# Kernel optimization log

Measured on AMD Instinct MI355X. Metric: run time of the kernel, lower is better.

Reference implementation:

```python
import math
import jax, jax.numpy as jnp
import numpy as np

S, B, H, D = 2048, 1, 16, 128  # seq, batch, heads, head_dim (hard-coded in source)
COEFF = 1.0  # layer_num = 1
NORM_FACTOR = math.sqrt(2048 / 16) * COEFF  # sqrt(HIDDEN/NUM_HEADS) * coeff


def setup_inputs() -> dict:
    key = jax.random.key(0)
    k1, k2, k3, k4, k5 = jax.random.split(key, 5)
    query_layer = jax.random.normal(k1, (S, B, H, D), dtype=jnp.float32)
    key_layer = jax.random.normal(k2, (S, B, H, D), dtype=jnp.float32)
    value_layer = jax.random.normal(k3, (S, B, H, D), dtype=jnp.float32)
    # causal mask, True = masked (Megatron convention)
    attention_mask = jnp.triu(jnp.ones((S, S), dtype=bool), k=1)[None, None]
    # per-head SVD right-singular-vector matrices (orthonormal-ish; random here)
    svd_qk = jax.random.normal(k4, (H, D, D), dtype=jnp.float32) / math.sqrt(D)
    svd_v = jax.random.normal(k5, (H, D, D), dtype=jnp.float32) / math.sqrt(D)
    return {"query_layer": query_layer, "key_layer": key_layer,
            "value_layer": value_layer, "attention_mask": attention_mask,
            "svd_qk": svd_qk, "svd_v": svd_v}


def reference(query_layer, key_layer, value_layer, attention_mask, svd_qk, svd_v):
    # q/k/v: [S, 1, H, D] -> project each head through its SVD matrix
    q = jnp.einsum('shd,hde->hse', query_layer[:, 0], svd_qk)  # [H,S,D]
    k = jnp.einsum('shd,hde->hse', key_layer[:, 0], svd_qk)    # [H,S,D]
    # qk_drop = 0 -> h_mask zeroing of columns is a no-op (faithfully skipped)
    scores = jnp.einsum('hqe,hke->hqk', q, k) / NORM_FACTOR    # [H,S,S]
    mask = attention_mask[0, 0]                                 # [S,S] bool
    scores = jnp.where(mask, jnp.float32(-10000.0), scores)
    # FusedScaleMaskSoftmax: scale by coeff, re-mask, softmax
    scaled = jnp.where(mask, jnp.float32(-10000.0), scores * COEFF)
    probs = jax.nn.softmax(scaled, axis=-1)                     # [H,S,S]
    # attention dropout is identity in eval mode
    v = jnp.einsum('shd,hde->hse', value_layer[:, 0], svd_v)    # [H,S,D]
    # vlinear_drop = 0 -> column zeroing is a no-op
    ctx = jnp.einsum('hqk,hke->qhe', probs, v)                  # [S,H,D]
    return ctx.reshape(S, B, H * D)                             # [S,1,2048]
```

## Files before the change

### kernel.cpp

```cpp
#include <hip/hip_runtime.h>
#include <hip/hip_bf16.h>
#include <math.h>

#define S_LEN 2048
#define NHEAD 16
#define DHEAD 128

typedef __attribute__((ext_vector_type(8)))  _Float16 f16x8;
typedef __attribute__((ext_vector_type(4)))  _Float16 f16x4;
typedef __attribute__((ext_vector_type(4)))  float    f32x4;
typedef __attribute__((ext_vector_type(16))) float    f32x16;

__device__ __forceinline__ void permswap(unsigned &a, unsigned &b) {
    asm volatile("v_permlane32_swap_b32 %0, %1" : "+v"(a), "+v"(b));
}

typedef __attribute__((address_space(3))) unsigned int lds_u32;
typedef __attribute__((address_space(1))) const unsigned int glb_u32;
__device__ __forceinline__ void gload16(const void* g, void* l) {
    __builtin_amdgcn_global_load_lds((glb_u32*)g, (lds_u32*)l, 16, 0, 0);
}

__global__ __launch_bounds__(256) void transpose_w_kernel(
    const float* __restrict__ w_qk, const float* __restrict__ w_v,
    _Float16* __restrict__ wqk_t, _Float16* __restrict__ wv_t)
{
    __shared__ float tile[32][33];
    const int mat = blockIdx.z;
    const int h   = blockIdx.y;
    const int t0  = blockIdx.x;
    const int dt  = (t0 >> 2) * 32;
    const int et  = (t0 & 3) * 32;
    const float* src = (mat ? w_v : w_qk) + (size_t)h * DHEAD * DHEAD;
    _Float16*   dst = (mat ? wv_t : wqk_t) + (size_t)h * DHEAD * DHEAD;
    const int tx = threadIdx.x & 31, ty = threadIdx.x >> 5;
#pragma unroll
    for (int k = 0; k < 4; ++k)
        tile[ty + 8 * k][tx] = src[(size_t)(dt + ty + 8 * k) * DHEAD + et + tx];
    __syncthreads();
#pragma unroll
    for (int k = 0; k < 4; ++k)
        dst[(size_t)(et + ty + 8 * k) * DHEAD + dt + tx] = (_Float16)tile[tx][ty + 8 * k];
}

__global__ __launch_bounds__(256) void proj_kernel(
    const float* __restrict__ q_in, const float* __restrict__ k_in,
    const float* __restrict__ v_in,
    const _Float16* __restrict__ wqk_t, const _Float16* __restrict__ wv_t,
    _Float16* __restrict__ Qp, _Float16* __restrict__ Kp, _Float16* __restrict__ Vt)
{
    const int h   = blockIdx.x >> 5;
    const int rb  = blockIdx.x & 31;
    const int wv  = threadIdx.x >> 6;
    const int lane = threadIdx.x & 63;
    const int r16 = lane & 15;
    const int kg  = lane >> 4;
    const int s_base = rb * 64 + wv * 16;
    const int s_row  = s_base + r16;
    const float INV_NORM = 0.08838834764831845f;

    f16x8 aq[4], ak[4], av[4];
    {
        const float* qr = q_in + ((size_t)s_row * NHEAD + h) * DHEAD;
        const float* kr = k_in + ((size_t)s_row * NHEAD + h) * DHEAD;
        const float* vr = v_in + ((size_t)s_row * NHEAD + h) * DHEAD;
#pragma unroll
        for (int kb = 0; kb < 4; ++kb) {
            const int d0 = kb * 32 + kg * 8;
            const f32x4 q0 = *(const f32x4*)(qr + d0), q1 = *(const f32x4*)(qr + d0 + 4);
            const f32x4 k0 = *(const f32x4*)(kr + d0), k1 = *(const f32x4*)(kr + d0 + 4);
            const f32x4 v0 = *(const f32x4*)(vr + d0), v1 = *(const f32x4*)(vr + d0 + 4);
#pragma unroll
            for (int i = 0; i < 4; ++i) {
                aq[kb][i] = (_Float16)q0[i];  aq[kb][i + 4] = (_Float16)q1[i];
                ak[kb][i] = (_Float16)k0[i];  ak[kb][i + 4] = (_Float16)k1[i];
                av[kb][i] = (_Float16)v0[i];  av[kb][i + 4] = (_Float16)v1[i];
            }
        }
    }

    const _Float16* wq_h = wqk_t + (size_t)h * DHEAD * DHEAD;
    const _Float16* wv_h = wv_t  + (size_t)h * DHEAD * DHEAD;

#pragma unroll 2
    for (int cb = 0; cb < 8; ++cb) {
        f32x4 accq = {0.f, 0.f, 0.f, 0.f};
        f32x4 acck = {0.f, 0.f, 0.f, 0.f};
        f32x4 accv = {0.f, 0.f, 0.f, 0.f};
        const int c = cb * 16 + r16;
#pragma unroll
        for (int kb = 0; kb < 4; ++kb) {
            const f16x8 bqk = *(const f16x8*)(wq_h + (size_t)c * DHEAD + kb * 32 + kg * 8);
            const f16x8 bv  = *(const f16x8*)(wv_h + (size_t)c * DHEAD + kb * 32 + kg * 8);
            accq = __builtin_amdgcn_mfma_f32_16x16x32_f16(bqk, aq[kb], accq, 0, 0, 0);
            acck = __builtin_amdgcn_mfma_f32_16x16x32_f16(bqk, ak[kb], acck, 0, 0, 0);
            accv = __builtin_amdgcn_mfma_f32_16x16x32_f16(av[kb], bv,  accv, 0, 0, 0);
        }
        f16x4 qv, kv4;
#pragma unroll
        for (int jj = 0; jj < 4; ++jj) {
            qv[jj]  = (_Float16)(accq[jj] * INV_NORM);
            kv4[jj] = (_Float16)acck[jj];
        }
        *(f16x4*)(Qp + ((size_t)h * S_LEN + s_base + r16) * DHEAD + cb * 16 + kg * 4) = qv;
        *(f16x4*)(Kp + ((size_t)h * S_LEN + s_base + r16) * DHEAD + cb * 16 + kg * 4) = kv4;
        f16x4 vvv;
#pragma unroll
        for (int jj = 0; jj < 4; ++jj) vvv[jj] = (_Float16)accv[jj];
        *(f16x4*)(Vt + ((size_t)h * DHEAD + c) * S_LEN + s_base + kg * 4) = vvv;
    }
}

__device__ __forceinline__ void stage_k(const _Float16* kbase, _Float16* kst,
                                        int w, int lane, int par, int inext,
                                        int jmax_lock) {
#pragma unroll
    for (int cidx = 0; cidx < 2; ++cidx) {
        const int c      = 2 * w + cidx;
        const int role_c = c >> 3;
        const int cc     = c & 7;
        const int jn     = 2 * inext + role_c;
        if (jn < jmax_lock) {
            const int A    = cc * 1024 + lane * 16;
            const int srcO = A ^ (((A >> 8) & 15) << 4);
            const char* g  = (const char*)kbase + (size_t)jn * 8192 + srcO;
            char*       l  = (char*)kst + (size_t)(role_c * 2 + par) * 8192
                                        + cc * 1024;
            gload16(g, l);
        }
    }
}

__global__ __launch_bounds__(512, 2) void attn_kernel(
    const _Float16* __restrict__ Qp, const _Float16* __restrict__ Kp,
    const _Float16* __restrict__ Vt, float* __restrict__ out)
{
    __shared__ _Float16 Kst[4][4096];
    __shared__ _Float16 obuf[4][32][132];
    __shared__ float    mlbuf[4][2][32];

    const int h    = blockIdx.y;
    const int w    = threadIdx.x >> 6;
    const int lane = threadIdx.x & 63;
    const int q    = lane & 31;
    const int hi   = lane >> 5;

    const int qsub = w & 1;
    const int role = (w >> 1) & 1;
    const int tsel = w >> 2;
    const int t    = tsel ? (31 - blockIdx.x) : blockIdx.x;
    const int pairid = qsub + tsel * 2;
    const int q0w  = t * 64 + qsub * 32;
    const int jmax = 2 * t + 1 + qsub;
    const int q_abs = q0w + q;

    const int jmax_lock = 2 * (31 - blockIdx.x) + 2;
    const int I         = jmax_lock / 2;

    const _Float16* qbase = Qp + ((size_t)h * S_LEN + q0w) * DHEAD;
    const _Float16* kbase = Kp + (size_t)h * S_LEN * DHEAD;
    const _Float16* vbase = Vt + (size_t)h * DHEAD * S_LEN;

    const int lqk = q * DHEAD + hi * 8;
    const int lv  = q * S_LEN + hi * 8;
    const int swq = (q & 15) << 4;

    f16x8 qf[8];
#pragma unroll
    for (int m = 0; m < 8; ++m)
        qf[m] = *(const f16x8*)(qbase + lqk + m * 16);

    f32x16 acc[4];
#pragma unroll
    for (int e = 0; e < 4; ++e)
#pragma unroll
        for (int i = 0; i < 16; ++i) acc[e][i] = 0.f;

    float m_run = -1e30f, l_run = 0.f;

    stage_k(kbase, &Kst[0][0], w, lane, 0, 0, jmax_lock);

    int p = 0;
    for (int it = 0; it < I; ++it, p ^= 1) {
        __syncthreads();

        const int j   = 2 * it + role;
        const bool act = (j < jmax);
        const int kv0 = j * 32;

        f16x8 kf[8];
        if (act) {
            const char* kt = (const char*)&Kst[role * 2 + p][0];
#pragma unroll
            for (int m = 0; m < 8; ++m) {
                const int L = q * 256 + m * 32 + hi * 16;
                kf[m] = *(const f16x8*)(kt + (L ^ swq));
            }
        }

        if (it + 1 < I)
            stage_k(kbase, &Kst[0][0], w, lane, p ^ 1, it + 1, jmax_lock);

        if (act) {
            f32x16 s0, s1;
#pragma unroll
            for (int i = 0; i < 16; ++i) { s0[i] = 0.f; s1[i] = 0.f; }
#pragma unroll
            for (int m = 0; m < 8; m += 2) {
                s0 = __builtin_amdgcn_mfma_f32_32x32x16_f16(kf[m],     qf[m],     s0, 0, 0, 0);
                s1 = __builtin_amdgcn_mfma_f32_32x32x16_f16(kf[m + 1], qf[m + 1], s1, 0, 0, 0);
            }

            f16x8 vf[8];
#pragma unroll
            for (int e = 0; e < 4; ++e) {
                const _Float16* vp = vbase + (size_t)e * 32 * S_LEN + lv + kv0;
                vf[2 * e]     = *(const f16x8*)(vp);
                vf[2 * e + 1] = *(const f16x8*)(vp + 16);
            }

            f32x16 sv = s0 + s1;

            if (kv0 == q0w) {
#pragma unroll
                for (int i = 0; i < 16; ++i) {
                    const int krel = (i & 3) + 8 * (i >> 2) + 4 * hi;
                    if (kv0 + krel > q_abs) sv[i] = -1e30f;
                }
            }

            float t0 = fmaxf(sv[0], sv[1]),  t1 = fmaxf(sv[2], sv[3]);
            float t2 = fmaxf(sv[4], sv[5]),  t3 = fmaxf(sv[6], sv[7]);
            float t4 = fmaxf(sv[8], sv[9]),  t5 = fmaxf(sv[10], sv[11]);
            float t6 = fmaxf(sv[12], sv[13]), t7 = fmaxf(sv[14], sv[15]);
            t0 = fmaxf(t0, t1); t2 = fmaxf(t2, t3); t4 = fmaxf(t4, t5); t6 = fmaxf(t6, t7);
            float tm = fmaxf(fmaxf(t0, t2), fmaxf(t4, t6));
            tm = fmaxf(tm, __shfl_xor(tm, 32, 64));

            const float mnew = fmaxf(m_run, tm);
            if (__any(tm > m_run)) {
                const float corr = __expf(m_run - mnew);
                l_run *= corr;
#pragma unroll
                for (int e = 0; e < 4; ++e)
#pragma unroll
                    for (int i = 0; i < 16; ++i) acc[e][i] *= corr;
                m_run = mnew;
            }

#pragma unroll
            for (int i = 0; i < 16; ++i) sv[i] = __expf(sv[i] - m_run);
            float r0 = (sv[0] + sv[1]) + (sv[2] + sv[3]);
            float r1 = (sv[4] + sv[5]) + (sv[6] + sv[7]);
            float r2 = (sv[8] + sv[9]) + (sv[10] + sv[11]);
            float r3 = (sv[12] + sv[13]) + (sv[14] + sv[15]);
            float rs = (r0 + r1) + (r2 + r3);
            rs += __shfl_xor(rs, 32, 64);
            l_run += rs;

            unsigned u0 = __builtin_bit_cast(unsigned, __builtin_amdgcn_cvt_pkrtz(sv[0],  sv[1]));
            unsigned u1 = __builtin_bit_cast(unsigned, __builtin_amdgcn_cvt_pkrtz(sv[2],  sv[3]));
            unsigned u2 = __builtin_bit_cast(unsigned, __builtin_amdgcn_cvt_pkrtz(sv[4],  sv[5]));
            unsigned u3 = __builtin_bit_cast(unsigned, __builtin_amdgcn_cvt_pkrtz(sv[6],  sv[7]));
            unsigned u4 = __builtin_bit_cast(unsigned, __builtin_amdgcn_cvt_pkrtz(sv[8],  sv[9]));
            unsigned u5 = __builtin_bit_cast(unsigned, __builtin_amdgcn_cvt_pkrtz(sv[10], sv[11]));
            unsigned u6 = __builtin_bit_cast(unsigned, __builtin_amdgcn_cvt_pkrtz(sv[12], sv[13]));
            unsigned u7 = __builtin_bit_cast(unsigned, __builtin_amdgcn_cvt_pkrtz(sv[14], sv[15]));
            permswap(u0, u2); permswap(u1, u3);
            permswap(u4, u6); permswap(u5, u7);
            union uf8 { unsigned w[4]; f16x8 v; };
            uf8 p0; p0.w[0] = u0; p0.w[1] = u1; p0.w[2] = u2; p0.w[3] = u3;
            uf8 p1; p1.w[0] = u4; p1.w[1] = u5; p1.w[2] = u6; p1.w[3] = u7;

#pragma unroll
            for (int e = 0; e < 4; ++e) {
                acc[e] = __builtin_amdgcn_mfma_f32_32x32x16_f16(vf[2 * e],     p0.v, acc[e], 0, 0, 0);
                acc[e] = __builtin_amdgcn_mfma_f32_32x32x16_f16(vf[2 * e + 1], p1.v, acc[e], 0, 0, 0);
            }
        }
    }

    if (role) {
        if (hi == 0) { mlbuf[pairid][0][q] = m_run; mlbuf[pairid][1][q] = l_run; }
#pragma unroll
        for (int e = 0; e < 4; ++e)
#pragma unroll
            for (int i = 0; i < 16; ++i) {
                const int erow = e * 32 + (i & 3) + 8 * (i >> 2) + 4 * hi;
                obuf[pairid][q][erow] = (_Float16)acc[e][i];
            }
    }
    __syncthreads();
    if (!role) {
        const float mb = mlbuf[pairid][0][q];
        const float lb = mlbuf[pairid][1][q];
        const float ms = fmaxf(m_run, mb);
        const float ca = __expf(m_run - ms);
        const float cb = __expf(mb - ms);
        const float rinv = 1.0f / (l_run * ca + lb * cb);
        float* orow = out + (size_t)q_abs * (NHEAD * DHEAD) + h * DHEAD;
#pragma unroll
        for (int e = 0; e < 4; ++e) {
#pragma unroll
            for (int g = 0; g < 4; ++g) {
                f32x4 vv;
#pragma unroll
                for (int c = 0; c < 4; ++c) {
                    const int i = g * 4 + c;
                    const int erow = e * 32 + 8 * g + 4 * hi + c;
                    vv[c] = (acc[e][i] * ca + (float)obuf[pairid][q][erow] * cb) * rinv;
                }
                *(f32x4*)(orow + e * 32 + 8 * g + 4 * hi) = vv;
            }
        }
    }
}

extern "C" void kernel_launch(void* const* d_in, const int* in_sizes, int n_in,
                              void* d_out, int out_size, void* d_ws, size_t ws_size,
                              hipStream_t stream) {
    const float* q_in = (const float*)d_in[0];
    const float* k_in = (const float*)d_in[1];
    const float* v_in = (const float*)d_in[2];
    const float* w_qk = (const float*)d_in[4];
    const float* w_v  = (const float*)d_in[5];
    float* out = (float*)d_out;

    const size_t mat_elems = (size_t)NHEAD * S_LEN * DHEAD;
    const size_t w_elems   = (size_t)NHEAD * DHEAD * DHEAD;
    _Float16* Qp   = (_Float16*)d_ws;
    _Float16* Kp   = Qp + mat_elems;
    _Float16* Vt   = Kp + mat_elems;
    _Float16* Wqkt = Vt + mat_elems;
    _Float16* Wvt  = Wqkt + w_elems;

    transpose_w_kernel<<<dim3(16, NHEAD, 2), dim3(256), 0, stream>>>(w_qk, w_v, Wqkt, Wvt);
    proj_kernel<<<dim3(NHEAD * 32), dim3(256), 0, stream>>>(q_in, k_in, v_in, Wqkt, Wvt, Qp, Kp, Vt);
    attn_kernel<<<dim3(16, NHEAD), dim3(512), 0, stream>>>(Qp, Kp, Vt, out);
}
```

Measured before the change: 92.44 us.

## Process two KV tiles per iteration per role and use exp2 softmax

Each wave now handles two 32-key tiles per loop iteration, and the K staging buffer grows to eight slots so each step loads four tiles. This halves the number of barriers and online-softmax rescale checks. The 1/sqrt(d) scale now includes log2(e), so the softmax uses exp2f instead of __expf. In exchange, LDS use and register pressure go up, which could lower occupancy at 2 blocks per CU, and the tile-granularity masking becomes a little coarser.

```diff
diff --git a/kernel.cpp b/kernel.cpp
--- a/kernel.cpp
+++ b/kernel.cpp
@@ -57,7 +57,7 @@
     const int kg  = lane >> 4;
     const int s_base = rb * 64 + wv * 16;
     const int s_row  = s_base + r16;
-    const float INV_NORM = 0.08838834764831845f;
+    const float INV_NORM = 0.12752211758f;
 
     f16x8 aq[4], ak[4], av[4];
     {
@@ -111,20 +111,20 @@
     }
 }
 
-__device__ __forceinline__ void stage_k(const _Float16* kbase, _Float16* kst,
-                                        int w, int lane, int par, int inext,
-                                        int jmax_lock) {
-#pragma unroll
-    for (int cidx = 0; cidx < 2; ++cidx) {
-        const int c      = 2 * w + cidx;
-        const int role_c = c >> 3;
-        const int cc     = c & 7;
-        const int jn     = 2 * inext + role_c;
+__device__ __forceinline__ void stage_k4(const _Float16* kbase, _Float16* kst,
+                                         int w, int lane, int par, int inext,
+                                         int jmax_lock) {
+#pragma unroll
+    for (int cidx = 0; cidx < 4; ++cidx) {
+        const int c    = 4 * w + cidx;
+        const int slot = c >> 3;
+        const int cc   = c & 7;
+        const int jn   = 4 * inext + slot;
         if (jn < jmax_lock) {
             const int A    = cc * 1024 + lane * 16;
             const int srcO = A ^ (((A >> 8) & 15) << 4);
             const char* g  = (const char*)kbase + (size_t)jn * 8192 + srcO;
-            char*       l  = (char*)kst + (size_t)(role_c * 2 + par) * 8192
+            char*       l  = (char*)kst + (size_t)(slot * 2 + par) * 8192
                                         + cc * 1024;
             gload16(g, l);
         }
@@ -135,7 +135,7 @@
     const _Float16* __restrict__ Qp, const _Float16* __restrict__ Kp,
     const _Float16* __restrict__ Vt, float* __restrict__ out)
 {
-    __shared__ _Float16 Kst[4][4096];
+    __shared__ _Float16 Kst[8][4096];
     __shared__ _Float16 obuf[4][32][132];
     __shared__ float    mlbuf[4][2][32];
 
@@ -155,7 +155,7 @@
     const int q_abs = q0w + q;
 
     const int jmax_lock = 2 * (31 - blockIdx.x) + 2;
-    const int I         = jmax_lock / 2;
+    const int I         = (jmax_lock + 3) >> 2;
 
     const _Float16* qbase = Qp + ((size_t)h * S_LEN + q0w) * DHEAD;
     const _Float16* kbase = Kp + (size_t)h * S_LEN * DHEAD;
@@ -178,68 +178,108 @@
 
     float m_run = -1e30f, l_run = 0.f;
 
-    stage_k(kbase, &Kst[0][0], w, lane, 0, 0, jmax_lock);
+    stage_k4(kbase, &Kst[0][0], w, lane, 0, 0, jmax_lock);
 
     int p = 0;
     for (int it = 0; it < I; ++it, p ^= 1) {
         __syncthreads();
 
-        const int j   = 2 * it + role;
-        const bool act = (j < jmax);
-        const int kv0 = j * 32;
-
-        f16x8 kf[8];
-        if (act) {
-            const char* kt = (const char*)&Kst[role * 2 + p][0];
+        const int jA = 4 * it + 2 * role;
+        const int jB = jA + 1;
+        const bool actA = (jA < jmax);
+        const bool actB = (jB < jmax);
+
+        if (it + 1 < I)
+            stage_k4(kbase, &Kst[0][0], w, lane, p ^ 1, it + 1, jmax_lock);
+
+        if (actA) {
+            const int kv0A = jA * 32;
+            const int kv0B = jB * 32;
+            const char* ktA = (const char*)&Kst[(2 * role) * 2 + p][0];
+            const char* ktB = (const char*)&Kst[(2 * role + 1) * 2 + p][0];
+
+            f16x8 kfA[8];
 #pragma unroll
             for (int m = 0; m < 8; ++m) {
                 const int L = q * 256 + m * 32 + hi * 16;
-                kf[m] = *(const f16x8*)(kt + (L ^ swq));
-            }
-        }
-
-        if (it + 1 < I)
-            stage_k(kbase, &Kst[0][0], w, lane, p ^ 1, it + 1, jmax_lock);
-
-        if (act) {
-            f32x16 s0, s1;
-#pragma unroll
-            for (int i = 0; i < 16; ++i) { s0[i] = 0.f; s1[i] = 0.f; }
+                kfA[m] = *(const f16x8*)(ktA + (L ^ swq));
+            }
+            f32x16 s0A, s1A;
+#pragma unroll
+            for (int i = 0; i < 16; ++i) { s0A[i] = 0.f; s1A[i] = 0.f; }
 #pragma unroll
             for (int m = 0; m < 8; m += 2) {
-                s0 = __builtin_amdgcn_mfma_f32_32x32x16_f16(kf[m],     qf[m],     s0, 0, 0, 0);
-                s1 = __builtin_amdgcn_mfma_f32_32x32x16_f16(kf[m + 1], qf[m + 1], s1, 0, 0, 0);
-            }
-
-            f16x8 vf[8];
+                s0A = __builtin_amdgcn_mfma_f32_32x32x16_f16(kfA[m],     qf[m],     s0A, 0, 0, 0);
+                s1A = __builtin_amdgcn_mfma_f32_32x32x16_f16(kfA[m + 1], qf[m + 1], s1A, 0, 0, 0);
+            }
+
+            f16x8 kfB[8];
+#pragma unroll
+            for (int m = 0; m < 8; ++m) {
+                const int L = q * 256 + m * 32 + hi * 16;
+                kfB[m] = *(const f16x8*)(ktB + (L ^ swq));
+            }
+            f32x16 s0B, s1B;
+#pragma unroll
+            for (int i = 0; i < 16; ++i) { s0B[i] = 0.f; s1B[i] = 0.f; }
+#pragma unroll
+            for (int m = 0; m < 8; m += 2) {
+                s0B = __builtin_amdgcn_mfma_f32_32x32x16_f16(kfB[m],     qf[m],     s0B, 0, 0, 0);
+                s1B = __builtin_amdgcn_mfma_f32_32x32x16_f16(kfB[m + 1], qf[m + 1], s1B, 0, 0, 0);
+            }
+
+            f16x8 vfA[8];
 #pragma unroll
             for (int e = 0; e < 4; ++e) {
-                const _Float16* vp = vbase + (size_t)e * 32 * S_LEN + lv + kv0;
-                vf[2 * e]     = *(const f16x8*)(vp);
-                vf[2 * e + 1] = *(const f16x8*)(vp + 16);
-            }
-
-            f32x16 sv = s0 + s1;
-
-            if (kv0 == q0w) {
+                const _Float16* vp = vbase + (size_t)e * 32 * S_LEN + lv + kv0A;
+                vfA[2 * e]     = *(const f16x8*)(vp);
+                vfA[2 * e + 1] = *(const f16x8*)(vp + 16);
+            }
+
+            f32x16 svA = s0A + s1A;
+            if (kv0A == q0w) {
 #pragma unroll
                 for (int i = 0; i < 16; ++i) {
                     const int krel = (i & 3) + 8 * (i >> 2) + 4 * hi;
-                    if (kv0 + krel > q_abs) sv[i] = -1e30f;
+                    if (kv0A + krel > q_abs) svA[i] = -1e30f;
                 }
             }
 
-            float t0 = fmaxf(sv[0], sv[1]),  t1 = fmaxf(sv[2], sv[3]);
-            float t2 = fmaxf(sv[4], sv[5]),  t3 = fmaxf(sv[6], sv[7]);
-            float t4 = fmaxf(sv[8], sv[9]),  t5 = fmaxf(sv[10], sv[11]);
-            float t6 = fmaxf(sv[12], sv[13]), t7 = fmaxf(sv[14], sv[15]);
-            t0 = fmaxf(t0, t1); t2 = fmaxf(t2, t3); t4 = fmaxf(t4, t5); t6 = fmaxf(t6, t7);
-            float tm = fmaxf(fmaxf(t0, t2), fmaxf(t4, t6));
+            f16x8 vfB[8];
+#pragma unroll
+            for (int e = 0; e < 4; ++e) {
+                const _Float16* vp = vbase + (size_t)e * 32 * S_LEN + lv + kv0B;
+                vfB[2 * e]     = *(const f16x8*)(vp);
+                vfB[2 * e + 1] = *(const f16x8*)(vp + 16);
+            }
+
+            f32x16 svB;
+#pragma unroll
+            for (int i = 0; i < 16; ++i)
+                svB[i] = actB ? (s0B[i] + s1B[i]) : -1e30f;
+            if (actB && kv0B == q0w) {
+#pragma unroll
+                for (int i = 0; i < 16; ++i) {
+                    const int krel = (i & 3) + 8 * (i >> 2) + 4 * hi;
+                    if (kv0B + krel > q_abs) svB[i] = -1e30f;
+                }
+            }
+
+            float a0 = fmaxf(fmaxf(svA[0], svA[1]),   fmaxf(svA[2], svA[3]));
+            float a1 = fmaxf(fmaxf(svA[4], svA[5]),   fmaxf(svA[6], svA[7]));
+            float a2 = fmaxf(fmaxf(svA[8], svA[9]),   fmaxf(svA[10], svA[11]));
+            float a3 = fmaxf(fmaxf(svA[12], svA[13]), fmaxf(svA[14], svA[15]));
+            float b0 = fmaxf(fmaxf(svB[0], svB[1]),   fmaxf(svB[2], svB[3]));
+            float b1 = fmaxf(fmaxf(svB[4], svB[5]),   fmaxf(svB[6], svB[7]));
+            float b2 = fmaxf(fmaxf(svB[8], svB[9]),   fmaxf(svB[10], svB[11]));
+            float b3 = fmaxf(fmaxf(svB[12], svB[13]), fmaxf(svB[14], svB[15]));
+            float tm = fmaxf(fmaxf(fmaxf(a0, a1), fmaxf(a2, a3)),
+                             fmaxf(fmaxf(b0, b1), fmaxf(b2, b3)));
             tm = fmaxf(tm, __shfl_xor(tm, 32, 64));
 
-            const float mnew = fmaxf(m_run, tm);
             if (__any(tm > m_run)) {
-                const float corr = __expf(m_run - mnew);
+                const float mnew = fmaxf(m_run, tm);
+                const float corr = exp2f(m_run - mnew);
                 l_run *= corr;
 #pragma unroll
                 for (int e = 0; e < 4; ++e)
@@ -249,34 +289,57 @@
             }
 
 #pragma unroll
-            for (int i = 0; i < 16; ++i) sv[i] = __expf(sv[i] - m_run);
-            float r0 = (sv[0] + sv[1]) + (sv[2] + sv[3]);
-            float r1 = (sv[4] + sv[5]) + (sv[6] + sv[7]);
-            float r2 = (sv[8] + sv[9]) + (sv[10] + sv[11]);
-            float r3 = (sv[12] + sv[13]) + (sv[14] + sv[15]);
-            float rs = (r0 + r1) + (r2 + r3);
+            for (int i = 0; i < 16; ++i) svA[i] = exp2f(svA[i] - m_run);
+            unsigned uA0 = __builtin_bit_cast(unsigned, __builtin_amdgcn_cvt_pkrtz(svA[0],  svA[1]));
+            unsigned uA1 = __builtin_bit_cast(unsigned, __builtin_amdgcn_cvt_pkrtz(svA[2],  svA[3]));
+            unsigned uA2 = __builtin_bit_cast(unsigned, __builtin_amdgcn_cvt_pkrtz(svA[4],  svA[5]));
+            unsigned uA3 = __builtin_bit_cast(unsigned, __builtin_amdgcn_cvt_pkrtz(svA[6],  svA[7]));
+            unsigned uA4 = __builtin_bit_cast(unsigned, __builtin_amdgcn_cvt_pkrtz(svA[8],  svA[9]));
+            unsigned uA5 = __builtin_bit_cast(unsigned, __builtin_amdgcn_cvt_pkrtz(svA[10], svA[11]));
+            unsigned uA6 = __builtin_bit_cast(unsigned, __builtin_amdgcn_cvt_pkrtz(svA[12], svA[13]));
+            unsigned uA7 = __builtin_bit_cast(unsigned, __builtin_amdgcn_cvt_pkrtz(svA[14], svA[15]));
+            permswap(uA0, uA2); permswap(uA1, uA3);
+            permswap(uA4, uA6); permswap(uA5, uA7);
+            union uf8 { unsigned w[4]; f16x8 v; };
+            uf8 pA0; pA0.w[0] = uA0; pA0.w[1] = uA1; pA0.w[2] = uA2; pA0.w[3] = uA3;
+            uf8 pA1; pA1.w[0] = uA4; pA1.w[1] = uA5; pA1.w[2] = uA6; pA1.w[3] = uA7;
+#pragma unroll
+            for (int e = 0; e < 4; ++e) {
+                acc[e] = __builtin_amdgcn_mfma_f32_32x32x16_f16(vfA[2 * e],     pA0.v, acc[e], 0, 0, 0);
+                acc[e] = __builtin_amdgcn_mfma_f32_32x32x16_f16(vfA[2 * e + 1], pA1.v, acc[e], 0, 0, 0);
+            }
+
+#pragma unroll
+            for (int i = 0; i < 16; ++i) svB[i] = exp2f(svB[i] - m_run);
+            unsigned uB0 = __builtin_bit_cast(unsigned, __builtin_amdgcn_cvt_pkrtz(svB[0],  svB[1]));
+            unsigned uB1 = __builtin_bit_cast(unsigned, __builtin_amdgcn_cvt_pkrtz(svB[2],  svB[3]));
+            unsigned uB2 = __builtin_bit_cast(unsigned, __builtin_amdgcn_cvt_pkrtz(svB[4],  svB[5]));
+            unsigned uB3 = __builtin_bit_cast(unsigned, __builtin_amdgcn_cvt_pkrtz(svB[6],  svB[7]));
+            unsigned uB4 = __builtin_bit_cast(unsigned, __builtin_amdgcn_cvt_pkrtz(svB[8],  svB[9]));
+            unsigned uB5 = __builtin_bit_cast(unsigned, __builtin_amdgcn_cvt_pkrtz(svB[10], svB[11]));
+            unsigned uB6 = __builtin_bit_cast(unsigned, __builtin_amdgcn_cvt_pkrtz(svB[12], svB[13]));
+            unsigned uB7 = __builtin_bit_cast(unsigned, __builtin_amdgcn_cvt_pkrtz(svB[14], svB[15]));
+            permswap(uB0, uB2); permswap(uB1, uB3);
+            permswap(uB4, uB6); permswap(uB5, uB7);
+            uf8 pB0; pB0.w[0] = uB0; pB0.w[1] = uB1; pB0.w[2] = uB2; pB0.w[3] = uB3;
+            uf8 pB1; pB1.w[0] = uB4; pB1.w[1] = uB5; pB1.w[2] = uB6; pB1.w[3] = uB7;
+#pragma unroll
+            for (int e = 0; e < 4; ++e) {
+                acc[e] = __builtin_amdgcn_mfma_f32_32x32x16_f16(vfB[2 * e],     pB0.v, acc[e], 0, 0, 0);
+                acc[e] = __builtin_amdgcn_mfma_f32_32x32x16_f16(vfB[2 * e + 1], pB1.v, acc[e], 0, 0, 0);
+            }
+
+            float rA = ((svA[0] + svA[1]) + (svA[2] + svA[3]))
+                     + ((svA[4] + svA[5]) + (svA[6] + svA[7]))
+                     + ((svA[8] + svA[9]) + (svA[10] + svA[11]))
+                     + ((svA[12] + svA[13]) + (svA[14] + svA[15]));
+            float rB = ((svB[0] + svB[1]) + (svB[2] + svB[3]))
+                     + ((svB[4] + svB[5]) + (svB[6] + svB[7]))
+                     + ((svB[8] + svB[9]) + (svB[10] + svB[11]))
+                     + ((svB[12] + svB[13]) + (svB[14] + svB[15]));
+            float rs = rA + rB;
             rs += __shfl_xor(rs, 32, 64);
             l_run += rs;
-
-            unsigned u0 = __builtin_bit_cast(unsigned, __builtin_amdgcn_cvt_pkrtz(sv[0],  sv[1]));
-            unsigned u1 = __builtin_bit_cast(unsigned, __builtin_amdgcn_cvt_pkrtz(sv[2],  sv[3]));
-            unsigned u2 = __builtin_bit_cast(unsigned, __builtin_amdgcn_cvt_pkrtz(sv[4],  sv[5]));
-            unsigned u3 = __builtin_bit_cast(unsigned, __builtin_amdgcn_cvt_pkrtz(sv[6],  sv[7]));
-            unsigned u4 = __builtin_bit_cast(unsigned, __builtin_amdgcn_cvt_pkrtz(sv[8],  sv[9]));
-            unsigned u5 = __builtin_bit_cast(unsigned, __builtin_amdgcn_cvt_pkrtz(sv[10], sv[11]));
-            unsigned u6 = __builtin_bit_cast(unsigned, __builtin_amdgcn_cvt_pkrtz(sv[12], sv[13]));
-            unsigned u7 = __builtin_bit_cast(unsigned, __builtin_amdgcn_cvt_pkrtz(sv[14], sv[15]));
-            permswap(u0, u2); permswap(u1, u3);
-            permswap(u4, u6); permswap(u5, u7);
-            union uf8 { unsigned w[4]; f16x8 v; };
-            uf8 p0; p0.w[0] = u0; p0.w[1] = u1; p0.w[2] = u2; p0.w[3] = u3;
-            uf8 p1; p1.w[0] = u4; p1.w[1] = u5; p1.w[2] = u6; p1.w[3] = u7;
-
-#pragma unroll
-            for (int e = 0; e < 4; ++e) {
-                acc[e] = __builtin_amdgcn_mfma_f32_32x32x16_f16(vf[2 * e],     p0.v, acc[e], 0, 0, 0);
-                acc[e] = __builtin_amdgcn_mfma_f32_32x32x16_f16(vf[2 * e + 1], p1.v, acc[e], 0, 0, 0);
-            }
         }
     }
 
@@ -295,8 +358,8 @@
         const float mb = mlbuf[pairid][0][q];
         const float lb = mlbuf[pairid][1][q];
         const float ms = fmaxf(m_run, mb);
-        const float ca = __expf(m_run - ms);
-        const float cb = __expf(mb - ms);
+        const float ca = exp2f(m_run - ms);
+        const float cb = exp2f(mb - ms);
         const float rinv = 1.0f / (l_run * ca + lb * cb);
         float* orow = out + (size_t)q_abs * (NHEAD * DHEAD) + h * DHEAD;
 #pragma unroll
```

Measured after the change: 95.76 us. 1.04x slower.
